# Kernel optimization log

Hardware: AMD Instinct MI355X
Metric: run time of the kernel (lower is better)

The kernel has to match this reference:

```python
import jax, jax.numpy as jnp
import numpy as np

FACTOR = 5

def _prob_attention(queries, keys, values):
    # queries/keys/values: [B, L, H, D]
    B, L_Q, H, D = queries.shape
    L_K = keys.shape[1]
    q = jnp.transpose(queries, (0, 2, 1, 3))  # [B,H,L_Q,D]
    k = jnp.transpose(keys, (0, 2, 1, 3))
    v = jnp.transpose(values, (0, 2, 1, 3))

    U_part = min(FACTOR * int(np.ceil(np.log(L_K))), L_K)  # sample_k
    u = min(FACTOR * int(np.ceil(np.log(L_Q))), L_Q)       # n_top

    # random K sampling (fixed key -> deterministic reference)
    skey = jax.random.key(42)
    index_sample = jax.random.randint(skey, (L_Q, U_part), 0, L_K)  # [L_Q, S]
    K_sample = k[:, :, index_sample, :]  # [B,H,L_Q,S,D]
    Q_K_sample = jnp.einsum('bhqd,bhqsd->bhqs', q, K_sample)  # [B,H,L_Q,S]

    # sparsity measure and top-u query selection
    M = jnp.max(Q_K_sample, axis=-1) - jnp.mean(Q_K_sample, axis=-1)  # [B,H,L_Q]
    _, M_top = jax.lax.top_k(M, u)  # [B,H,u]

    Q_reduce = jnp.take_along_axis(q, M_top[..., None], axis=2)  # [B,H,u,D]
    scores = jnp.einsum('bhud,bhkd->bhuk', Q_reduce, k)  # [B,H,u,L_K]
    scale = 1.0 / jnp.sqrt(jnp.asarray(D, dtype=q.dtype))
    scores = scores * scale

    # initial context: mean of V over keys, tiled over queries (mask_flag=False)
    V_mean = jnp.mean(v, axis=-2, keepdims=True)  # [B,H,1,D]
    context = jnp.broadcast_to(V_mean, (B, H, L_Q, D))

    attn = jax.nn.softmax(scores, axis=-1)  # [B,H,u,L_K]
    update = jnp.einsum('bhuk,bhkd->bhud', attn, v)  # [B,H,u,D]

    # scatter updates into context at selected query positions
    bi = jnp.arange(B)[:, None, None]
    hi = jnp.arange(H)[None, :, None]
    context = context.at[bi, hi, M_top].set(update)

    return jnp.transpose(context, (0, 2, 1, 3))  # [B,L_Q,H,D]


def setup_inputs() -> dict:
    key = jax.random.key(0)
    kq, kk, kv = jax.random.split(key, 3)
    B, L, H, D = 4, 2048, 8, 64
    return {
        'queries': jax.random.normal(kq, (B, L, H, D), dtype=jnp.float32),
        'keys': jax.random.normal(kk, (B, L, H, D), dtype=jnp.float32),
        'values': jax.random.normal(kv, (B, L, H, D), dtype=jnp.float32),
        'attn_mask': jnp.zeros((1,), dtype=jnp.bool_),  # unused (mask_flag=False)
    }


def reference(queries, keys, values, attn_mask):
    context = _prob_attention(queries, keys, values)
    return context
```

## Files before the change

kernel.cpp:

```cpp
#include <hip/hip_runtime.h>
#include <hip/hip_bf16.h>
#include <math.h>
#include <stdint.h>

static constexpr int BB = 4;
static constexpr int LL = 2048;
static constexpr int HH = 8;
static constexpr int DD = 64;
static constexpr int UU = 40;
static constexpr int NSAMP = 40;
static constexpr int BHL = BB * HH * LL;
static constexpr int ROWSTRIDE = HH * DD;
static constexpr int VCHUNKS = 64;
static constexpr int NC = 16;
static constexpr int CR = 128;
static constexpr int QS = 20;
static constexpr int SCOREBLK = BHL / 4;
static constexpr int P1BLK = SCOREBLK + BB * HH * VCHUNKS;

static constexpr size_t WS_NEED = 5682176;

__device__ __forceinline__ uint32_t rotl32(uint32_t x, uint32_t n) {
  return (x << n) | (x >> (32u - n));
}

__device__ __forceinline__ void tf2x32(uint32_t k0, uint32_t k1,
                                       uint32_t x0, uint32_t x1,
                                       uint32_t& o0, uint32_t& o1) {
  uint32_t ks[3] = {k0, k1, k0 ^ k1 ^ 0x1BD11BDAu};
  x0 += ks[0];
  x1 += ks[1];
  const uint32_t rotA[4] = {13u, 15u, 26u, 6u};
  const uint32_t rotB[4] = {17u, 29u, 16u, 24u};
#pragma unroll
  for (int i = 0; i < 5; ++i) {
    const uint32_t* r = (i & 1) ? rotB : rotA;
#pragma unroll
    for (int j = 0; j < 4; ++j) {
      x0 += x1;
      x1 = rotl32(x1, r[j]);
      x1 ^= x0;
    }
    x0 += ks[(i + 1) % 3];
    x1 += ks[(i + 2) % 3] + (uint32_t)(i + 1);
  }
  o0 = x0;
  o1 = x1;
}

__device__ __forceinline__ float dot4(float4 a, float4 b) {
  return a.x * b.x + a.y * b.y + a.z * b.z + a.w * b.w;
}

__global__ void __launch_bounds__(256)
k_phase1(const float* __restrict__ q, const float* __restrict__ k,
         const float* __restrict__ v, float* __restrict__ M,
         float* __restrict__ vpart) {
  if (blockIdx.x < SCOREBLK) {
    int wg = (blockIdx.x & 7) * (SCOREBLK / 8) + (blockIdx.x >> 3);
    int w = wg * 4 + (threadIdx.x >> 6);
    int lane = threadIdx.x & 63;
    int qq = w & (LL - 1);
    int h = (w >> 11) & (HH - 1);
    int b = w >> 14;
    uint32_t ka, kb;
    tf2x32(0u, 42u, 0u, 1u, ka, kb);
    uint32_t o0, o1;
    tf2x32(ka, kb, 0u, (uint32_t)(qq * NSAMP + lane), o0, o1);
    int idxv = (int)((o0 ^ o1) & 2047u);
    int rr = lane >> 3;
    int dc = lane & 7;
    const float* qrow = q + (((size_t)b * LL + qq) * HH + h) * DD;
    float4 q0 = ((const float4*)qrow)[dc * 2];
    float4 q1 = ((const float4*)qrow)[dc * 2 + 1];
    const float* kbase = k + ((size_t)b * LL * HH + h) * DD;
    int kr[5];
#pragma unroll
    for (int it = 0; it < 5; ++it) kr[it] = __shfl(idxv, it * 8 + rr);
    float4 kva[5], kvb[5];
#pragma unroll
    for (int it = 0; it < 5; ++it) {
      const float4* kp = (const float4*)(kbase + (size_t)kr[it] * ROWSTRIDE);
      kva[it] = kp[dc * 2];
      kvb[it] = kp[dc * 2 + 1];
    }
    float mx = -1.0e30f, sm = 0.0f;
#pragma unroll
    for (int it = 0; it < 5; ++it) {
      float p = dot4(q0, kva[it]) + dot4(q1, kvb[it]);
      p += __shfl_xor(p, 1);
      p += __shfl_xor(p, 2);
      p += __shfl_xor(p, 4);
      mx = fmaxf(mx, p);
      sm += p;
    }
#pragma unroll
    for (int off = 8; off <= 32; off <<= 1) {
      mx = fmaxf(mx, __shfl_xor(mx, off));
      sm += __shfl_xor(sm, off);
    }
    if (lane == 0) M[w] = mx - sm * (1.0f / (float)NSAMP);
  } else {
    __shared__ float part[4][DD];
    int bid = blockIdx.x - SCOREBLK;
    int bh = bid >> 6;
    int chunk = bid & 63;
    int b = bh >> 3, h = bh & 7;
    int t = threadIdx.x;
    int wv = t >> 6, lane = t & 63;
    int l0 = chunk * (LL / VCHUNKS);
    const float* base = v + ((size_t)b * LL * HH + h) * DD + lane;
    float s = 0.0f;
#pragma unroll
    for (int r = wv; r < LL / VCHUNKS; r += 4) s += base[(size_t)(l0 + r) * ROWSTRIDE];
    part[wv][lane] = s;
    __syncthreads();
    if (t < DD) {
      vpart[(size_t)bid * DD + t] =
          (part[0][t] + part[1][t]) + (part[2][t] + part[3][t]);
    }
  }
}

__global__ void __launch_bounds__(256)
k_phase2(const float* __restrict__ M, const float* __restrict__ vpart,
         int* __restrict__ mtop, float* __restrict__ vmean, int* __restrict__ tbl) {
  if (blockIdx.x < BB * HH) {
    __shared__ uint32_t keys[LL];
    __shared__ int hist[256];
    __shared__ int scan_res[2];
    __shared__ int nsel, neq;
    __shared__ int sel[UU];
    __shared__ int eqlist[64];
    int bh = blockIdx.x;
    int t = threadIdx.x;
    const float* m = M + (size_t)bh * LL;
    for (int i = t; i < LL; i += 256) {
      uint32_t u = __float_as_uint(m[i]);
      keys[i] = (u & 0x80000000u) ? ~u : (u | 0x80000000u);
      tbl[bh * LL + i] = -1;
    }
    if (t == 0) { nsel = 0; neq = 0; }
    __syncthreads();

    uint32_t prefix = 0, prefmask = 0;
    int remaining = UU;
#pragma unroll
    for (int shift = 24; shift >= 0; shift -= 8) {
      hist[t] = 0;
      __syncthreads();
      for (int i = t; i < LL; i += 256) {
        uint32_t kk = keys[i];
        if ((kk & prefmask) == prefix) atomicAdd(&hist[(kk >> shift) & 0xFF], 1);
      }
      __syncthreads();
      if (t < 64) {
        int b0 = t * 4;
        int c0 = hist[b0], c1 = hist[b0 + 1], c2 = hist[b0 + 2], c3 = hist[b0 + 3];
        int g = c0 + c1 + c2 + c3;
        int s = g;
#pragma unroll
        for (int off = 1; off < 64; off <<= 1) {
          int o = __shfl_down(s, off);
          if (t + off < 64) s += o;
        }
        int a3 = s - g;
        int a2 = a3 + c3;
        int a1 = a2 + c2;
        int a0 = a1 + c1;
        if (a3 < remaining && remaining <= a3 + c3) { scan_res[0] = b0 + 3; scan_res[1] = a3; }
        if (a2 < remaining && remaining <= a2 + c2) { scan_res[0] = b0 + 2; scan_res[1] = a2; }
        if (a1 < remaining && remaining <= a1 + c1) { scan_res[0] = b0 + 1; scan_res[1] = a1; }
        if (a0 < remaining && remaining <= a0 + c0) { scan_res[0] = b0 + 0; scan_res[1] = a0; }
      }
      __syncthreads();
      prefix |= ((uint32_t)scan_res[0] << shift);
      prefmask |= (0xFFu << shift);
      remaining -= scan_res[1];
      __syncthreads();
    }

    uint32_t T = prefix;
    for (int i = t; i < LL; i += 256) {
      uint32_t kk = keys[i];
      if (kk > T) {
        int p = atomicAdd(&nsel, 1);
        sel[p] = i;
      } else if (kk == T) {
        int p = atomicAdd(&neq, 1);
        if (p < 64) eqlist[p] = i;
      }
    }
    __syncthreads();
    if (t == 0) {
      int need = UU - nsel;
      int count = neq < 64 ? neq : 64;
      for (int r = 0; r < need; ++r) {
        int mn = 1 << 30, mpos = 0;
        for (int e = 0; e < count; ++e)
          if (eqlist[e] < mn) { mn = eqlist[e]; mpos = e; }
        sel[nsel + r] = mn;
        eqlist[mpos] = 1 << 30;
      }
    }
    __syncthreads();
    if (t < UU) {
      mtop[bh * UU + t] = sel[t];
      tbl[bh * LL + sel[t]] = t;
    }
  } else {
    int bh = blockIdx.x - BB * HH;
    int d = threadIdx.x;
    if (d < DD) {
      const float* p = vpart + (size_t)bh * VCHUNKS * DD + d;
      float s = 0.0f;
#pragma unroll
      for (int c = 0; c < VCHUNKS; ++c) s += p[(size_t)c * DD];
      vmean[bh * DD + d] = s * (1.0f / (float)LL);
    }
  }
}

__global__ void __launch_bounds__(256)
k_attn_part(const float* __restrict__ q, const float* __restrict__ k,
            const float* __restrict__ v, const int* __restrict__ mtop,
            float* __restrict__ pm, float* __restrict__ ps,
            float* __restrict__ pacc) {
  __shared__ float qs_[QS][DD];
  __shared__ float sc[QS][CR];
  int blk = blockIdx.x;
  int c = blk & (NC - 1);
  int qh = (blk >> 4) & 1;
  int bh = blk >> 5;
  int b = bh >> 3, h = bh & 7;
  int t = threadIdx.x;
  int wv = t >> 6, lane = t & 63;
  int l0 = c * CR;
  int j0 = qh * QS;

  for (int i = t; i < QS * DD; i += 256) {
    int jj = i >> 6, d = i & 63;
    int l = mtop[bh * UU + j0 + jj];
    qs_[jj][d] = q[(((size_t)b * LL + l) * HH + h) * DD + d];
  }
  __syncthreads();

  const float* kbase = k + ((size_t)b * LL * HH + h) * DD;
  int rr = lane & 15, dcq = lane >> 4;
  float4 kv0[4], kv1[4];
  {
    const float* kr0 = kbase + (size_t)(l0 + wv * 32 + rr) * ROWSTRIDE + dcq * 16;
    const float* kr1 = kbase + (size_t)(l0 + wv * 32 + 16 + rr) * ROWSTRIDE + dcq * 16;
#pragma unroll
    for (int i = 0; i < 4; ++i) {
      kv0[i] = *(const float4*)(kr0 + i * 4);
      kv1[i] = *(const float4*)(kr1 + i * 4);
    }
  }
#pragma unroll 4
  for (int jj = 0; jj < QS; ++jj) {
    const float* qp = &qs_[jj][dcq * 16];
    float4 qa = *(const float4*)(qp);
    float4 qb = *(const float4*)(qp + 4);
    float4 qc = *(const float4*)(qp + 8);
    float4 qd = *(const float4*)(qp + 12);
    float p0 = dot4(qa, kv0[0]) + dot4(qb, kv0[1]) + dot4(qc, kv0[2]) + dot4(qd, kv0[3]);
    float p1 = dot4(qa, kv1[0]) + dot4(qb, kv1[1]) + dot4(qc, kv1[2]) + dot4(qd, kv1[3]);
    p0 += __shfl_xor(p0, 16);
    p0 += __shfl_xor(p0, 32);
    p1 += __shfl_xor(p1, 16);
    p1 += __shfl_xor(p1, 32);
    if (lane < 16) {
      sc[jj][wv * 32 + lane] = p0 * 0.125f;
      sc[jj][wv * 32 + 16 + lane] = p1 * 0.125f;
    }
  }
  __syncthreads();

#pragma unroll
  for (int u = 0; u < 5; ++u) {
    int jj = wv * 5 + u;
    float a0 = sc[jj][lane];
    float a1 = sc[jj][lane + 64];
    float mx = fmaxf(a0, a1);
#pragma unroll
    for (int off = 32; off; off >>= 1) mx = fmaxf(mx, __shfl_xor(mx, off));
    float e0 = expf(a0 - mx), e1 = expf(a1 - mx);
    sc[jj][lane] = e0;
    sc[jj][lane + 64] = e1;
    float s = e0 + e1;
#pragma unroll
    for (int off = 32; off; off >>= 1) s += __shfl_xor(s, off);
    if (lane == 0) {
      pm[(size_t)(bh * NC + c) * UU + j0 + jj] = mx;
      ps[(size_t)(bh * NC + c) * UU + j0 + jj] = s;
    }
  }
  const float* vbase = v + ((size_t)b * LL * HH + h) * DD + lane;
  float acc[5] = {0.f, 0.f, 0.f, 0.f, 0.f};
  for (int r = 0; r < CR; r += 4) {
    float v0 = vbase[(size_t)(l0 + r + 0) * ROWSTRIDE];
    float v1 = vbase[(size_t)(l0 + r + 1) * ROWSTRIDE];
    float v2 = vbase[(size_t)(l0 + r + 2) * ROWSTRIDE];
    float v3 = vbase[(size_t)(l0 + r + 3) * ROWSTRIDE];
#pragma unroll
    for (int u = 0; u < 5; ++u) {
      float4 p4 = *(const float4*)&sc[wv * 5 + u][r];
      acc[u] += p4.x * v0 + p4.y * v1 + p4.z * v2 + p4.w * v3;
    }
  }
#pragma unroll
  for (int u = 0; u < 5; ++u) {
    pacc[((size_t)(bh * NC + c) * UU + j0 + wv * 5 + u) * DD + lane] = acc[u];
  }
}

__global__ void __launch_bounds__(256)
k_out(const float* __restrict__ pm, const float* __restrict__ ps,
      const float* __restrict__ pacc, const int* __restrict__ tbl,
      const float* __restrict__ vmean, float* __restrict__ out) {
  int wid = (blockIdx.x * 256 + threadIdx.x) >> 6;
  int lane = threadIdx.x & 63;
  int l = wid & (LL - 1);
  int bh = wid >> 11;
  int b = bh >> 3, h = bh & 7;
  int j = tbl[bh * LL + l];
  float* orow = out + (((size_t)b * LL + l) * HH + h) * DD;
  if (j < 0) {
    orow[lane] = vmean[bh * DD + lane];
  } else {
    float mv = (lane < NC) ? pm[(size_t)(bh * NC + lane) * UU + j] : -1.0e30f;
    float mx = mv;
#pragma unroll
    for (int off = 32; off; off >>= 1) mx = fmaxf(mx, __shfl_xor(mx, off));
    float e = (lane < NC) ? expf(mv - mx) : 0.0f;
    float sv = (lane < NC) ? ps[(size_t)(bh * NC + lane) * UU + j] * e : 0.0f;
    float st = sv;
#pragma unroll
    for (int off = 32; off; off >>= 1) st += __shfl_xor(st, off);
    float a = 0.0f;
#pragma unroll
    for (int c2 = 0; c2 < NC; ++c2) {
      float ec = __shfl(e, c2);
      a += ec * pacc[((size_t)(bh * NC + c2) * UU + j) * DD + lane];
    }
    orow[lane] = a / st;
  }
}

__global__ void k_fill(const float* __restrict__ vmean, float* __restrict__ out) {
  int f = blockIdx.x * 256 + threadIdx.x;
  int d4 = f & 15;
  int h = (f >> 4) & 7;
  int b = f >> 18;
  ((float4*)out)[f] = ((const float4*)vmean)[(((b << 3) + h) << 4) + d4];
}

__global__ void k_attn_mono(const float* __restrict__ q, const float* __restrict__ k,
                            const float* __restrict__ v, const int* __restrict__ mtop,
                            float* __restrict__ out) {
  __shared__ float sc[LL];
  __shared__ float redm[4];
  __shared__ float reds[4];
  __shared__ float redp[4][DD];
  int blk = blockIdx.x;
  int j = blk % UU;
  int bh = blk / UU;
  int b = bh >> 3, h = bh & 7;
  int l = mtop[bh * UU + j];
  int t = threadIdx.x;
  int wv = t >> 6, lane = t & 63;
  int dc = t & 15, r2 = (t >> 4) & 3;
  const float4* qrow = (const float4*)(q + (((size_t)b * LL + l) * HH + h) * DD);
  float4 qv = qrow[dc];
  const float* kbase = k + ((size_t)b * LL * HH + h) * DD;
#pragma unroll 4
  for (int base = wv * 4; base < LL; base += 16) {
    int row = base + r2;
    const float4* krow = (const float4*)(kbase + (size_t)row * ROWSTRIDE);
    float4 kv = krow[dc];
    float p = dot4(qv, kv);
    p += __shfl_xor(p, 1);
    p += __shfl_xor(p, 2);
    p += __shfl_xor(p, 4);
    p += __shfl_xor(p, 8);
    if (dc == 0) sc[row] = p * 0.125f;
  }
  __syncthreads();
  const float4* sc4 = (const float4*)sc;
  float4 ea0 = sc4[t];
  float4 ea1 = sc4[t + 256];
  float mx = fmaxf(fmaxf(fmaxf(ea0.x, ea0.y), fmaxf(ea0.z, ea0.w)),
                   fmaxf(fmaxf(ea1.x, ea1.y), fmaxf(ea1.z, ea1.w)));
#pragma unroll
  for (int off = 32; off; off >>= 1) mx = fmaxf(mx, __shfl_xor(mx, off));
  if (lane == 0) redm[wv] = mx;
  __syncthreads();
  mx = fmaxf(fmaxf(redm[0], redm[1]), fmaxf(redm[2], redm[3]));
  ea0.x = expf(ea0.x - mx); ea0.y = expf(ea0.y - mx);
  ea0.z = expf(ea0.z - mx); ea0.w = expf(ea0.w - mx);
  ea1.x = expf(ea1.x - mx); ea1.y = expf(ea1.y - mx);
  ea1.z = expf(ea1.z - mx); ea1.w = expf(ea1.w - mx);
  float psum = ((ea0.x + ea0.y) + (ea0.z + ea0.w)) + ((ea1.x + ea1.y) + (ea1.z + ea1.w));
  float4* sc4w = (float4*)sc;
  sc4w[t] = ea0;
  sc4w[t + 256] = ea1;
#pragma unroll
  for (int off = 32; off; off >>= 1) psum += __shfl_xor(psum, off);
  if (lane == 0) reds[wv] = psum;
  __syncthreads();
  float inv = 1.0f / ((reds[0] + reds[1]) + (reds[2] + reds[3]));
  const float* vbase = v + ((size_t)b * LL * HH + h) * DD + lane;
  float acc = 0.0f;
#pragma unroll 2
  for (int base = wv * 4; base < LL; base += 16) {
    float4 p4 = sc4[base >> 2];
    acc += p4.x * vbase[(size_t)(base + 0) * ROWSTRIDE];
    acc += p4.y * vbase[(size_t)(base + 1) * ROWSTRIDE];
    acc += p4.z * vbase[(size_t)(base + 2) * ROWSTRIDE];
    acc += p4.w * vbase[(size_t)(base + 3) * ROWSTRIDE];
  }
  redp[wv][lane] = acc;
  __syncthreads();
  if (t < DD) {
    float r = (redp[0][t] + redp[1][t]) + (redp[2][t] + redp[3][t]);
    out[(((size_t)b * LL + l) * HH + h) * DD + t] = r * inv;
  }
}

extern "C" void kernel_launch(void* const* d_in, const int* in_sizes, int n_in,
                              void* d_out, int out_size, void* d_ws, size_t ws_size,
                              hipStream_t stream) {
  const float* q = (const float*)d_in[0];
  const float* k = (const float*)d_in[1];
  const float* v = (const float*)d_in[2];
  float* out = (float*)d_out;
  char* ws = (char*)d_ws;

  if (ws_size >= WS_NEED) {
    float* M = (float*)(ws);
    float* vpart = (float*)(ws + 262144);
    float* pm = (float*)(ws);
    float* ps = (float*)(ws + 81920);
    float* pacc = (float*)(ws + 163840);
    int* mtop = (int*)(ws + 5406720);
    float* vmean = (float*)(ws + 5411840);
    int* tbl = (int*)(ws + 5420032);

    k_phase1<<<P1BLK, 256, 0, stream>>>(q, k, v, M, vpart);
    k_phase2<<<2 * BB * HH, 256, 0, stream>>>(M, vpart, mtop, vmean, tbl);
    k_attn_part<<<BB * HH * NC * 2, 256, 0, stream>>>(q, k, v, mtop, pm, ps, pacc);
    k_out<<<BHL / 4, 256, 0, stream>>>(pm, ps, pacc, tbl, vmean, out);
  } else {
    float* M = (float*)(ws);
    int* tbl = (int*)(ws);
    float* vpart = (float*)(ws + 262144);
    int* mtop = (int*)(ws + 786432);
    float* vmean = (float*)(ws + 791552);

    k_phase1<<<P1BLK, 256, 0, stream>>>(q, k, v, M, vpart);
    k_phase2<<<2 * BB * HH, 256, 0, stream>>>(M, vpart, mtop, vmean, tbl);
    k_fill<<<(BB * LL * HH * DD / 4) / 256, 256, 0, stream>>>(vmean, out);
    k_attn_mono<<<BB * HH * UU, 256, 0, stream>>>(q, k, v, mtop, out);
  }
}
```

Baseline: 170.7 us.

## Precompute random sample indices once and split key-row work across waves in attention

The threefry index generation moves out of the per-(b,h,q) scoring kernel into a pre-pass that writes the L*NSAMP sample indices once. A separate scoring kernel then reads them, so the hash is no longer recomputed 32 times per index. In k_attn_part, each wave now accumulates all 20 queries over a quarter of the key rows instead of 5 queries over all rows, so each wave loads each V row only once. The partial results are reduced through shared memory. The cost is an extra kernel launch, an extra global round-trip for the indices, and 20 accumulators per thread plus an 20KB shared buffer, which may reduce occupancy.

```diff
diff --git a/kernel.cpp b/kernel.cpp
--- a/kernel.cpp
+++ b/kernel.cpp
@@ -10,13 +10,15 @@
 static constexpr int UU = 40;
 static constexpr int NSAMP = 40;
 static constexpr int BHL = BB * HH * LL;
+static constexpr int NIDX = LL * NSAMP;
 static constexpr int ROWSTRIDE = HH * DD;
 static constexpr int VCHUNKS = 64;
 static constexpr int NC = 16;
 static constexpr int CR = 128;
 static constexpr int QS = 20;
 static constexpr int SCOREBLK = BHL / 4;
-static constexpr int P1BLK = SCOREBLK + BB * HH * VCHUNKS;
+static constexpr int IDXBLK = NIDX / 256;
+static constexpr int PREBLK = IDXBLK + BB * HH * VCHUNKS;
 
 static constexpr size_t WS_NEED = 5682176;
 
@@ -53,56 +55,17 @@
 }
 
 __global__ void __launch_bounds__(256)
-k_phase1(const float* __restrict__ q, const float* __restrict__ k,
-         const float* __restrict__ v, float* __restrict__ M,
-         float* __restrict__ vpart) {
-  if (blockIdx.x < SCOREBLK) {
-    int wg = (blockIdx.x & 7) * (SCOREBLK / 8) + (blockIdx.x >> 3);
-    int w = wg * 4 + (threadIdx.x >> 6);
-    int lane = threadIdx.x & 63;
-    int qq = w & (LL - 1);
-    int h = (w >> 11) & (HH - 1);
-    int b = w >> 14;
+k_pre(const float* __restrict__ v, int* __restrict__ idx, float* __restrict__ vpart) {
+  if (blockIdx.x < IDXBLK) {
+    int i = blockIdx.x * 256 + threadIdx.x;
     uint32_t ka, kb;
     tf2x32(0u, 42u, 0u, 1u, ka, kb);
     uint32_t o0, o1;
-    tf2x32(ka, kb, 0u, (uint32_t)(qq * NSAMP + lane), o0, o1);
-    int idxv = (int)((o0 ^ o1) & 2047u);
-    int rr = lane >> 3;
-    int dc = lane & 7;
-    const float* qrow = q + (((size_t)b * LL + qq) * HH + h) * DD;
-    float4 q0 = ((const float4*)qrow)[dc * 2];
-    float4 q1 = ((const float4*)qrow)[dc * 2 + 1];
-    const float* kbase = k + ((size_t)b * LL * HH + h) * DD;
-    int kr[5];
-#pragma unroll
-    for (int it = 0; it < 5; ++it) kr[it] = __shfl(idxv, it * 8 + rr);
-    float4 kva[5], kvb[5];
-#pragma unroll
-    for (int it = 0; it < 5; ++it) {
-      const float4* kp = (const float4*)(kbase + (size_t)kr[it] * ROWSTRIDE);
-      kva[it] = kp[dc * 2];
-      kvb[it] = kp[dc * 2 + 1];
-    }
-    float mx = -1.0e30f, sm = 0.0f;
-#pragma unroll
-    for (int it = 0; it < 5; ++it) {
-      float p = dot4(q0, kva[it]) + dot4(q1, kvb[it]);
-      p += __shfl_xor(p, 1);
-      p += __shfl_xor(p, 2);
-      p += __shfl_xor(p, 4);
-      mx = fmaxf(mx, p);
-      sm += p;
-    }
-#pragma unroll
-    for (int off = 8; off <= 32; off <<= 1) {
-      mx = fmaxf(mx, __shfl_xor(mx, off));
-      sm += __shfl_xor(sm, off);
-    }
-    if (lane == 0) M[w] = mx - sm * (1.0f / (float)NSAMP);
+    tf2x32(ka, kb, 0u, (uint32_t)i, o0, o1);
+    idx[i] = (int)((o0 ^ o1) & 2047u);
   } else {
     __shared__ float part[4][DD];
-    int bid = blockIdx.x - SCOREBLK;
+    int bid = blockIdx.x - IDXBLK;
     int bh = bid >> 6;
     int chunk = bid & 63;
     int b = bh >> 3, h = bh & 7;
@@ -120,6 +83,50 @@
           (part[0][t] + part[1][t]) + (part[2][t] + part[3][t]);
     }
   }
+}
+
+__global__ void __launch_bounds__(256)
+k_scores(const float* __restrict__ q, const float* __restrict__ k,
+         const int* __restrict__ idx, float* __restrict__ M) {
+  int wg = (blockIdx.x & 7) * (SCOREBLK / 8) + (blockIdx.x >> 3);
+  int w = wg * 4 + (threadIdx.x >> 6);
+  int lane = threadIdx.x & 63;
+  int qq = w & (LL - 1);
+  int h = (w >> 11) & (HH - 1);
+  int b = w >> 14;
+  int idxv = (lane < NSAMP) ? idx[qq * NSAMP + lane] : 0;
+  int rr = lane >> 3;
+  int dc = lane & 7;
+  const float* qrow = q + (((size_t)b * LL + qq) * HH + h) * DD;
+  float4 q0 = ((const float4*)qrow)[dc * 2];
+  float4 q1 = ((const float4*)qrow)[dc * 2 + 1];
+  const float* kbase = k + ((size_t)b * LL * HH + h) * DD;
+  int kr[5];
+#pragma unroll
+  for (int it = 0; it < 5; ++it) kr[it] = __shfl(idxv, it * 8 + rr);
+  float4 kva[5], kvb[5];
+#pragma unroll
+  for (int it = 0; it < 5; ++it) {
+    const float4* kp = (const float4*)(kbase + (size_t)kr[it] * ROWSTRIDE);
+    kva[it] = kp[dc * 2];
+    kvb[it] = kp[dc * 2 + 1];
+  }
+  float mx = -1.0e30f, sm = 0.0f;
+#pragma unroll
+  for (int it = 0; it < 5; ++it) {
+    float p = dot4(q0, kva[it]) + dot4(q1, kvb[it]);
+    p += __shfl_xor(p, 1);
+    p += __shfl_xor(p, 2);
+    p += __shfl_xor(p, 4);
+    mx = fmaxf(mx, p);
+    sm += p;
+  }
+#pragma unroll
+  for (int off = 8; off <= 32; off <<= 1) {
+    mx = fmaxf(mx, __shfl_xor(mx, off));
+    sm += __shfl_xor(sm, off);
+  }
+  if (lane == 0) M[w] = mx - sm * (1.0f / (float)NSAMP);
 }
 
 __global__ void __launch_bounds__(256)
@@ -228,6 +235,7 @@
             float* __restrict__ pacc) {
   __shared__ float qs_[QS][DD];
   __shared__ float sc[QS][CR];
+  __shared__ float pl[4][QS][DD];
   int blk = blockIdx.x;
   int c = blk & (NC - 1);
   int qh = (blk >> 4) & 1;
@@ -296,22 +304,31 @@
       ps[(size_t)(bh * NC + c) * UU + j0 + jj] = s;
     }
   }
+  __syncthreads();
+
   const float* vbase = v + ((size_t)b * LL * HH + h) * DD + lane;
-  float acc[5] = {0.f, 0.f, 0.f, 0.f, 0.f};
-  for (int r = 0; r < CR; r += 4) {
+  float acc[QS];
+#pragma unroll
+  for (int u = 0; u < QS; ++u) acc[u] = 0.0f;
+  for (int r = wv * 32; r < wv * 32 + 32; r += 4) {
     float v0 = vbase[(size_t)(l0 + r + 0) * ROWSTRIDE];
     float v1 = vbase[(size_t)(l0 + r + 1) * ROWSTRIDE];
     float v2 = vbase[(size_t)(l0 + r + 2) * ROWSTRIDE];
     float v3 = vbase[(size_t)(l0 + r + 3) * ROWSTRIDE];
 #pragma unroll
-    for (int u = 0; u < 5; ++u) {
-      float4 p4 = *(const float4*)&sc[wv * 5 + u][r];
+    for (int u = 0; u < QS; ++u) {
+      float4 p4 = *(const float4*)&sc[u][r];
       acc[u] += p4.x * v0 + p4.y * v1 + p4.z * v2 + p4.w * v3;
     }
   }
 #pragma unroll
+  for (int u = 0; u < QS; ++u) pl[wv][u][lane] = acc[u];
+  __syncthreads();
+#pragma unroll
   for (int u = 0; u < 5; ++u) {
-    pacc[((size_t)(bh * NC + c) * UU + j0 + wv * 5 + u) * DD + lane] = acc[u];
+    int jj = wv * 5 + u;
+    float r = (pl[0][jj][lane] + pl[1][jj][lane]) + (pl[2][jj][lane] + pl[3][jj][lane]);
+    pacc[((size_t)(bh * NC + c) * UU + j0 + jj) * DD + lane] = r;
   }
 }
 
@@ -438,8 +455,9 @@
   char* ws = (char*)d_ws;
 
   if (ws_size >= WS_NEED) {
-    float* M = (float*)(ws);
-    float* vpart = (float*)(ws + 262144);
+    int* idx = (int*)(ws);
+    float* vpart = (float*)(ws + 327680);
+    float* M = (float*)(ws + 851968);
     float* pm = (float*)(ws);
     float* ps = (float*)(ws + 81920);
     float* pacc = (float*)(ws + 163840);
@@ -447,18 +465,21 @@
     float* vmean = (float*)(ws + 5411840);
     int* tbl = (int*)(ws + 5420032);
 
-    k_phase1<<<P1BLK, 256, 0, stream>>>(q, k, v, M, vpart);
+    k_pre<<<PREBLK, 256, 0, stream>>>(v, idx, vpart);
+    k_scores<<<SCOREBLK, 256, 0, stream>>>(q, k, idx, M);
     k_phase2<<<2 * BB * HH, 256, 0, stream>>>(M, vpart, mtop, vmean, tbl);
     k_attn_part<<<BB * HH * NC * 2, 256, 0, stream>>>(q, k, v, mtop, pm, ps, pacc);
     k_out<<<BHL / 4, 256, 0, stream>>>(pm, ps, pacc, tbl, vmean, out);
   } else {
-    float* M = (float*)(ws);
-    int* tbl = (int*)(ws);
-    float* vpart = (float*)(ws + 262144);
-    int* mtop = (int*)(ws + 786432);
-    float* vmean = (float*)(ws + 791552);
-
-    k_phase1<<<P1BLK, 256, 0, stream>>>(q, k, v, M, vpart);
+    int* idx = (int*)(ws);
+    float* vpart = (float*)(ws + 327680);
+    float* M = (float*)(ws + 851968);
+    int* mtop = (int*)(ws + 1114112);
+    float* vmean = (float*)(ws + 1119232);
+    int* tbl = (int*)(ws + 1127424);
+
+    k_pre<<<PREBLK, 256, 0, stream>>>(v, idx, vpart);
+    k_scores<<<SCOREBLK, 256, 0, stream>>>(q, k, idx, M);
     k_phase2<<<2 * BB * HH, 256, 0, stream>>>(M, vpart, mtop, vmean, tbl);
     k_fill<<<(BB * LL * HH * DD / 4) / 256, 256, 0, stream>>>(vmean, out);
     k_attn_mono<<<BB * HH * UU, 256, 0, stream>>>(q, k, v, mtop, out);
```

Result: faster. 165.8 us (-2.9%).
